# Optimization experiments

Measured on AMD Instinct MI355X. Metric: run time of the kernel, lower is better.

The kernel has to match this reference:

```python
import jax, jax.numpy as jnp
import numpy as np

EMBED_DIM = 256
MAX_SENT_NUM = 50


def position_embeddings(max_sent_num, embed_dim):
    # pos[p, i] = sin(p / 200**(i/embed_dim))
    p = jnp.arange(max_sent_num, dtype=jnp.float32)[:, None]
    i = jnp.arange(embed_dim, dtype=jnp.float32)[None, :] / embed_dim
    return jnp.sin(p / jnp.power(200.0, i))


def setup_inputs() -> dict:
    key = jax.random.key(0)
    k1, k2, k3, k4 = jax.random.split(key, 4)
    B, S, N, E = 8192, 50, 20, EMBED_DIM
    return {
        "encoded_sents": jax.random.normal(k1, (B, S, E), dtype=jnp.float32),
        "entities": jax.random.normal(k2, (B, N, E), dtype=jnp.float32),
        "attn_matrix": jax.random.normal(k3, (E, E), dtype=jnp.float32) * 0.05,
        "dense_w": jax.random.normal(k4, (E, 1), dtype=jnp.float32) * 0.05,
        "dense_b": jnp.zeros((1,), dtype=jnp.float32),
    }


def reference(encoded_sents, entities, attn_matrix, dense_w, dense_b):
    B, S, E = encoded_sents.shape
    pos = position_embeddings(MAX_SENT_NUM, E)[:S]          # [S, E]
    x = encoded_sents + pos[None, :, :]                      # [B, S, E]

    # attention over previous sentences; query = last sentence's hidden state
    query = x[:, -1, :]                                      # [B, E]
    logits = jnp.einsum("be,bse->bs", query, x)              # [B, S]
    coef = jax.nn.softmax(logits, axis=1)                    # [B, S]
    attn_hidden = jnp.einsum("bs,bse->be", coef, x)          # [B, E]

    # entity attention: (query @ W) elementwise-weighted sum over entities (no softmax)
    q_ent = attn_hidden @ attn_matrix                        # [B, E]
    attn_ent = jnp.einsum("be,bne->be", q_ent, entities)     # [B, E] (sum over n)

    return jax.nn.sigmoid(attn_ent @ dense_w + dense_b)      # [B, 1]
```

## Files before the change

kernel.cpp:

```cpp
#include <hip/hip_runtime.h>
#include <math.h>

#define BATCH 8192
#define SENTS 50
#define ED    256
#define NENT  20
#define BB    16

#define RATE_K 0.0298588132413075f

__global__ __launch_bounds__(256) void pos_kernel(float* __restrict__ pos_tab) {
    int s = blockIdx.x;
    int e = threadIdx.x;
    float rate = exp2f(-(float)e * RATE_K);
    pos_tab[s * ED + e] = sinf((float)s * rate);
}

__global__ __launch_bounds__(256) void ent_kernel(
    const float* __restrict__ entities, const float* __restrict__ dense_w,
    float* __restrict__ m_out)
{
    int t = threadIdx.x;
    int b = blockIdx.x * 4 + (t >> 6);
    int c = t & 63;

    const float4* e4 = (const float4*)(entities + (size_t)b * NENT * ED);

    float4 a[NENT];
    #pragma unroll
    for (int n = 0; n < NENT; ++n) a[n] = e4[n * 64 + c];

    float4 s = make_float4(0.f, 0.f, 0.f, 0.f);
    #pragma unroll
    for (int n = 0; n < NENT; ++n) {
        s.x += a[n].x; s.y += a[n].y; s.z += a[n].z; s.w += a[n].w;
    }

    float4 w4 = ((const float4*)dense_w)[c];
    s.x *= w4.x; s.y *= w4.y; s.z *= w4.z; s.w *= w4.w;
    ((float4*)(m_out + (size_t)b * ED))[c] = s;
}

__global__ __launch_bounds__(512) void attn_kernel(
    const float* __restrict__ sents, const float* __restrict__ pos_tab,
    float* __restrict__ h_out)
{
    __shared__ float logit_s[64];
    __shared__ float coef[64];
    __shared__ __align__(16) float4 part[8][64];

    int t  = threadIdx.x;
    int b  = blockIdx.x;
    int c  = t & 63;
    int sr = t >> 6;

    const float4* s4 = (const float4*)(sents + (size_t)b * SENTS * ED);
    const float4* p4 = (const float4*)pos_tab;

    bool has7 = (sr < 2);

    float4 xv[7], pv[7];
    #pragma unroll
    for (int k = 0; k < 6; ++k) xv[k] = s4[(sr + 8 * k) * 64 + c];
    float4 qsv = s4[49 * 64 + c];
    #pragma unroll
    for (int k = 0; k < 6; ++k) pv[k] = p4[(sr + 8 * k) * 64 + c];
    float4 qpv = p4[49 * 64 + c];
    if (has7) {
        xv[6] = s4[(sr + 48) * 64 + c];
        pv[6] = p4[(sr + 48) * 64 + c];
    }

    float4 x[7];
    #pragma unroll
    for (int k = 0; k < 6; ++k) {
        x[k].x = xv[k].x + pv[k].x; x[k].y = xv[k].y + pv[k].y;
        x[k].z = xv[k].z + pv[k].z; x[k].w = xv[k].w + pv[k].w;
    }
    if (has7) {
        x[6].x = xv[6].x + pv[6].x; x[6].y = xv[6].y + pv[6].y;
        x[6].z = xv[6].z + pv[6].z; x[6].w = xv[6].w + pv[6].w;
    } else {
        x[6] = make_float4(0.f, 0.f, 0.f, 0.f);
    }
    float4 q;
    q.x = qsv.x + qpv.x; q.y = qsv.y + qpv.y;
    q.z = qsv.z + qpv.z; q.w = qsv.w + qpv.w;

    #pragma unroll
    for (int k = 0; k < 7; ++k) {
        if (k < 6 || has7) {
            float4 v = x[k];
            float p = v.x * q.x + v.y * q.y + v.z * q.z + v.w * q.w;
            p += __shfl_down(p, 32);
            p += __shfl_down(p, 16);
            p += __shfl_down(p, 8);
            p += __shfl_down(p, 4);
            p += __shfl_down(p, 2);
            p += __shfl_down(p, 1);
            if (c == 0) logit_s[sr + 8 * k] = p;
        }
    }
    __syncthreads();

    if (sr == 0) {
        float l = (c < SENTS) ? logit_s[c] : -INFINITY;
        float mx = l;
        for (int off = 32; off >= 1; off >>= 1) mx = fmaxf(mx, __shfl_xor(mx, off));
        float ex = (c < SENTS) ? expf(l - mx) : 0.f;
        float sm = ex;
        for (int off = 32; off >= 1; off >>= 1) sm += __shfl_xor(sm, off);
        if (c < SENTS) coef[c] = ex / sm;
    }
    __syncthreads();

    float4 h = make_float4(0.f, 0.f, 0.f, 0.f);
    #pragma unroll
    for (int k = 0; k < 7; ++k) {
        if (k < 6 || has7) {
            float cf = coef[sr + 8 * k];
            h.x += cf * x[k].x; h.y += cf * x[k].y;
            h.z += cf * x[k].z; h.w += cf * x[k].w;
        }
    }
    part[sr][c] = h;
    __syncthreads();

    if (sr == 0) {
        float4 r = make_float4(0.f, 0.f, 0.f, 0.f);
        #pragma unroll
        for (int i = 0; i < 8; ++i) {
            float4 a = part[i][c];
            r.x += a.x; r.y += a.y; r.z += a.z; r.w += a.w;
        }
        ((float4*)(h_out + (size_t)b * ED))[c] = r;
    }
}

__global__ __launch_bounds__(256) void bilinear_kernel(
    const float* __restrict__ hws, const float* __restrict__ mws,
    const float* __restrict__ A, const float* __restrict__ dense_b,
    float* __restrict__ out)
{
    __shared__ __align__(16) float hl[BB][ED];
    __shared__ float ml[BB][ED];
    __shared__ float part[BB][ED];

    int t  = threadIdx.x;
    int b0 = blockIdx.x * BB;

    for (int i = 0; i < BB; ++i) {
        hl[i][t] = hws[(size_t)(b0 + i) * ED + t];
        ml[i][t] = mws[(size_t)(b0 + i) * ED + t];
    }
    __syncthreads();

    float acc[BB];
    #pragma unroll
    for (int i = 0; i < BB; ++i) acc[i] = 0.f;

    for (int ep = 0; ep < ED; ep += 4) {
        float a0 = A[(ep + 0) * ED + t];
        float a1 = A[(ep + 1) * ED + t];
        float a2 = A[(ep + 2) * ED + t];
        float a3 = A[(ep + 3) * ED + t];
        #pragma unroll
        for (int i = 0; i < BB; ++i) {
            float4 hv = *(const float4*)&hl[i][ep];
            acc[i] += hv.x * a0 + hv.y * a1 + hv.z * a2 + hv.w * a3;
        }
    }

    #pragma unroll
    for (int i = 0; i < BB; ++i) part[i][t] = acc[i] * ml[i][t];
    __syncthreads();

    int lane = t & 63, w = t >> 6;
    float bias = dense_b[0];
    for (int i = w; i < BB; i += 4) {
        float v = part[i][lane] + part[i][lane + 64] + part[i][lane + 128] + part[i][lane + 192];
        for (int off = 32; off >= 1; off >>= 1) v += __shfl_xor(v, off);
        if (lane == 0) out[b0 + i] = 1.f / (1.f + expf(-(v + bias)));
    }
}

__global__ __launch_bounds__(256) void fused_kernel(
    const float* __restrict__ sents, const float* __restrict__ entities,
    const float* __restrict__ A, const float* __restrict__ dense_w,
    const float* __restrict__ dense_b, float* __restrict__ out)
{
    __shared__ __align__(16) float xs[SENTS][ED + 4];
    __shared__ float logit_s[64];
    __shared__ float coef[64];
    __shared__ __align__(16) float harr[ED];
    __shared__ float marr[ED];
    __shared__ float red[4];

    int t    = threadIdx.x;
    int b    = blockIdx.x;
    int lane = t & 63;
    int w    = t >> 6;

    float rate = exp2f(-(float)t * RATE_K);
    const float* sp = sents + (size_t)b * SENTS * ED;
    for (int s = 0; s < SENTS; ++s)
        xs[s][t] = sp[s * ED + t] + sinf((float)s * rate);
    __syncthreads();

    float4 q = *(const float4*)&xs[SENTS - 1][lane * 4];
    for (int s = w; s < SENTS; s += 4) {
        float4 v = *(const float4*)&xs[s][lane * 4];
        float p = v.x * q.x + v.y * q.y + v.z * q.z + v.w * q.w;
        p += __shfl_down(p, 32);
        p += __shfl_down(p, 16);
        p += __shfl_down(p, 8);
        p += __shfl_down(p, 4);
        p += __shfl_down(p, 2);
        p += __shfl_down(p, 1);
        if (lane == 0) logit_s[s] = p;
    }
    __syncthreads();

    if (w == 0) {
        float l = (lane < SENTS) ? logit_s[lane] : -INFINITY;
        float mx = l;
        for (int off = 32; off >= 1; off >>= 1) mx = fmaxf(mx, __shfl_xor(mx, off));
        float ex = (lane < SENTS) ? expf(l - mx) : 0.f;
        float sm = ex;
        for (int off = 32; off >= 1; off >>= 1) sm += __shfl_xor(sm, off);
        if (lane < SENTS) coef[lane] = ex / sm;
    }
    __syncthreads();

    float h = 0.f;
    #pragma unroll
    for (int s = 0; s < SENTS; ++s) h += coef[s] * xs[s][t];

    const float* ent = entities + (size_t)b * NENT * ED;
    float es = 0.f;
    #pragma unroll
    for (int n = 0; n < NENT; ++n) es += ent[n * ED + t];
    float m = es * dense_w[t];

    harr[t] = h;
    marr[t] = m;
    __syncthreads();

    float acc = 0.f;
    for (int ep = 0; ep < ED; ep += 4) {
        float4 hv = *(const float4*)&harr[ep];
        acc += hv.x * A[(ep + 0) * ED + t];
        acc += hv.y * A[(ep + 1) * ED + t];
        acc += hv.z * A[(ep + 2) * ED + t];
        acc += hv.w * A[(ep + 3) * ED + t];
    }
    float val = acc * marr[t];
    val += __shfl_down(val, 32);
    val += __shfl_down(val, 16);
    val += __shfl_down(val, 8);
    val += __shfl_down(val, 4);
    val += __shfl_down(val, 2);
    val += __shfl_down(val, 1);
    if (lane == 0) red[w] = val;
    __syncthreads();
    if (t == 0) {
        float tot = red[0] + red[1] + red[2] + red[3];
        out[b] = 1.f / (1.f + expf(-(tot + dense_b[0])));
    }
}

extern "C" void kernel_launch(void* const* d_in, const int* in_sizes, int n_in,
                              void* d_out, int out_size, void* d_ws, size_t ws_size,
                              hipStream_t stream) {
    const float* sents    = (const float*)d_in[0];
    const float* entities = (const float*)d_in[1];
    const float* A        = (const float*)d_in[2];
    const float* dense_w  = (const float*)d_in[3];
    const float* dense_b  = (const float*)d_in[4];
    float* out = (float*)d_out;

    size_t pos_bytes = (size_t)SENTS * ED * sizeof(float);
    size_t hm_bytes  = (size_t)BATCH * ED * sizeof(float);
    size_t need = pos_bytes + 2 * hm_bytes;

    if (ws_size >= need) {
        float* pos_tab = (float*)d_ws;
        float* hws = (float*)((char*)d_ws + pos_bytes);
        float* mws = (float*)((char*)d_ws + pos_bytes + hm_bytes);
        pos_kernel<<<SENTS, ED, 0, stream>>>(pos_tab);
        ent_kernel<<<BATCH / 4, 256, 0, stream>>>(entities, dense_w, mws);
        attn_kernel<<<BATCH, 512, 0, stream>>>(sents, pos_tab, hws);
        bilinear_kernel<<<BATCH / BB, 256, 0, stream>>>(hws, mws, A, dense_b, out);
    } else {
        fused_kernel<<<BATCH, 256, 0, stream>>>(sents, entities, A, dense_w, dense_b, out);
    }
}
```

Baseline: 161.1 us.

## Fuse entity sum and position embedding into attention kernel

```diff
diff --git a/kernel.cpp b/kernel.cpp
--- a/kernel.cpp
+++ b/kernel.cpp
@@ -9,45 +9,15 @@
 
 #define RATE_K 0.0298588132413075f
 
-__global__ __launch_bounds__(256) void pos_kernel(float* __restrict__ pos_tab) {
-    int s = blockIdx.x;
-    int e = threadIdx.x;
-    float rate = exp2f(-(float)e * RATE_K);
-    pos_tab[s * ED + e] = sinf((float)s * rate);
-}
-
-__global__ __launch_bounds__(256) void ent_kernel(
-    const float* __restrict__ entities, const float* __restrict__ dense_w,
-    float* __restrict__ m_out)
-{
-    int t = threadIdx.x;
-    int b = blockIdx.x * 4 + (t >> 6);
-    int c = t & 63;
-
-    const float4* e4 = (const float4*)(entities + (size_t)b * NENT * ED);
-
-    float4 a[NENT];
-    #pragma unroll
-    for (int n = 0; n < NENT; ++n) a[n] = e4[n * 64 + c];
-
-    float4 s = make_float4(0.f, 0.f, 0.f, 0.f);
-    #pragma unroll
-    for (int n = 0; n < NENT; ++n) {
-        s.x += a[n].x; s.y += a[n].y; s.z += a[n].z; s.w += a[n].w;
-    }
-
-    float4 w4 = ((const float4*)dense_w)[c];
-    s.x *= w4.x; s.y *= w4.y; s.z *= w4.z; s.w *= w4.w;
-    ((float4*)(m_out + (size_t)b * ED))[c] = s;
-}
-
-__global__ __launch_bounds__(512) void attn_kernel(
-    const float* __restrict__ sents, const float* __restrict__ pos_tab,
-    float* __restrict__ h_out)
+__global__ __launch_bounds__(512, 6) void attn_ent_kernel(
+    const float* __restrict__ sents, const float* __restrict__ entities,
+    const float* __restrict__ dense_w,
+    float* __restrict__ h_out, float* __restrict__ m_out)
 {
     __shared__ float logit_s[64];
     __shared__ float coef[64];
     __shared__ __align__(16) float4 part[8][64];
+    __shared__ __align__(16) float4 parte[8][64];
 
     int t  = threadIdx.x;
     int b  = blockIdx.x;
@@ -55,37 +25,51 @@
     int sr = t >> 6;
 
     const float4* s4 = (const float4*)(sents + (size_t)b * SENTS * ED);
-    const float4* p4 = (const float4*)pos_tab;
+    const float4* e4 = (const float4*)(entities + (size_t)b * NENT * ED);
 
     bool has7 = (sr < 2);
 
-    float4 xv[7], pv[7];
+    float4 xv[7];
     #pragma unroll
     for (int k = 0; k < 6; ++k) xv[k] = s4[(sr + 8 * k) * 64 + c];
     float4 qsv = s4[49 * 64 + c];
-    #pragma unroll
-    for (int k = 0; k < 6; ++k) pv[k] = p4[(sr + 8 * k) * 64 + c];
-    float4 qpv = p4[49 * 64 + c];
-    if (has7) {
-        xv[6] = s4[(sr + 48) * 64 + c];
-        pv[6] = p4[(sr + 48) * 64 + c];
-    }
+    float4 ev0 = e4[(sr     ) * 64 + c];
+    float4 ev1 = e4[(sr +  8) * 64 + c];
+    float4 ev2 = make_float4(0.f, 0.f, 0.f, 0.f);
+    if (sr < 4) ev2 = e4[(sr + 16) * 64 + c];
+    if (has7) xv[6] = s4[(sr + 48) * 64 + c];
+
+    float4 rate;
+    rate.x = exp2f(-(float)(4 * c + 0) * RATE_K);
+    rate.y = exp2f(-(float)(4 * c + 1) * RATE_K);
+    rate.z = exp2f(-(float)(4 * c + 2) * RATE_K);
+    rate.w = exp2f(-(float)(4 * c + 3) * RATE_K);
+
+    float4 q;
+    q.x = qsv.x + __sinf(49.f * rate.x);
+    q.y = qsv.y + __sinf(49.f * rate.y);
+    q.z = qsv.z + __sinf(49.f * rate.z);
+    q.w = qsv.w + __sinf(49.f * rate.w);
 
     float4 x[7];
     #pragma unroll
-    for (int k = 0; k < 6; ++k) {
-        x[k].x = xv[k].x + pv[k].x; x[k].y = xv[k].y + pv[k].y;
-        x[k].z = xv[k].z + pv[k].z; x[k].w = xv[k].w + pv[k].w;
-    }
-    if (has7) {
-        x[6].x = xv[6].x + pv[6].x; x[6].y = xv[6].y + pv[6].y;
-        x[6].z = xv[6].z + pv[6].z; x[6].w = xv[6].w + pv[6].w;
-    } else {
-        x[6] = make_float4(0.f, 0.f, 0.f, 0.f);
-    }
-    float4 q;
-    q.x = qsv.x + qpv.x; q.y = qsv.y + qpv.y;
-    q.z = qsv.z + qpv.z; q.w = qsv.w + qpv.w;
+    for (int k = 0; k < 7; ++k) {
+        if (k < 6 || has7) {
+            float fs = (float)(sr + 8 * k);
+            x[k].x = xv[k].x + __sinf(fs * rate.x);
+            x[k].y = xv[k].y + __sinf(fs * rate.y);
+            x[k].z = xv[k].z + __sinf(fs * rate.z);
+            x[k].w = xv[k].w + __sinf(fs * rate.w);
+        } else {
+            x[k] = make_float4(0.f, 0.f, 0.f, 0.f);
+        }
+    }
+
+    float4 es;
+    es.x = ev0.x + ev1.x + ev2.x;
+    es.y = ev0.y + ev1.y + ev2.y;
+    es.z = ev0.z + ev1.z + ev2.z;
+    es.w = ev0.w + ev1.w + ev2.w;
 
     #pragma unroll
     for (int k = 0; k < 7; ++k) {
@@ -123,7 +107,8 @@
             h.z += cf * x[k].z; h.w += cf * x[k].w;
         }
     }
-    part[sr][c] = h;
+    part[sr][c]  = h;
+    parte[sr][c] = es;
     __syncthreads();
 
     if (sr == 0) {
@@ -134,6 +119,16 @@
             r.x += a.x; r.y += a.y; r.z += a.z; r.w += a.w;
         }
         ((float4*)(h_out + (size_t)b * ED))[c] = r;
+    } else if (sr == 1) {
+        float4 r = make_float4(0.f, 0.f, 0.f, 0.f);
+        #pragma unroll
+        for (int i = 0; i < 8; ++i) {
+            float4 a = parte[i][c];
+            r.x += a.x; r.y += a.y; r.z += a.z; r.w += a.w;
+        }
+        float4 w4 = ((const float4*)dense_w)[c];
+        r.x *= w4.x; r.y *= w4.y; r.z *= w4.z; r.w *= w4.w;
+        ((float4*)(m_out + (size_t)b * ED))[c] = r;
     }
 }
 
@@ -279,17 +274,13 @@
     const float* dense_b  = (const float*)d_in[4];
     float* out = (float*)d_out;
 
-    size_t pos_bytes = (size_t)SENTS * ED * sizeof(float);
-    size_t hm_bytes  = (size_t)BATCH * ED * sizeof(float);
-    size_t need = pos_bytes + 2 * hm_bytes;
+    size_t hm_bytes = (size_t)BATCH * ED * sizeof(float);
+    size_t need = 2 * hm_bytes;
 
     if (ws_size >= need) {
-        float* pos_tab = (float*)d_ws;
-        float* hws = (float*)((char*)d_ws + pos_bytes);
-        float* mws = (float*)((char*)d_ws + pos_bytes + hm_bytes);
-        pos_kernel<<<SENTS, ED, 0, stream>>>(pos_tab);
-        ent_kernel<<<BATCH / 4, 256, 0, stream>>>(entities, dense_w, mws);
-        attn_kernel<<<BATCH, 512, 0, stream>>>(sents, pos_tab, hws);
+        float* hws = (float*)d_ws;
+        float* mws = (float*)((char*)d_ws + hm_bytes);
+        attn_ent_kernel<<<BATCH, 512, 0, stream>>>(sents, entities, dense_w, hws, mws);
         bilinear_kernel<<<BATCH / BB, 256, 0, stream>>>(hws, mws, A, dense_b, out);
     } else {
         fused_kernel<<<BATCH, 256, 0, stream>>>(sents, entities, A, dense_w, dense_b, out);
```

Result: faster. 147.6 us (-8.4%).
